# Kernel optimization log

Measured on AMD Instinct MI355X. Metric: run time of the kernel, lower is better.

## Reference

```python
import jax, jax.numpy as jnp
import numpy as np

NODE, CLUSTER, IN_DIM, OUT_DIM = 2048, 32, 64, 64
BATCH = 32

def _xavier_uniform(key, shape):
    fan_in, fan_out = shape[0], shape[1]
    limit = float(np.sqrt(6.0 / (fan_in + fan_out)))
    return jax.random.uniform(key, shape, jnp.float32, -limit, limit)

def setup_inputs() -> dict:
    key = jax.random.key(0)
    k_a, k_h, k_al, k_be = jax.random.split(key, 4)
    a = jax.random.uniform(k_a, (BATCH, NODE, NODE), jnp.float32)
    h = jax.random.normal(k_h, (BATCH, NODE, IN_DIM), jnp.float32)
    alpha = _xavier_uniform(k_al, (NODE, CLUSTER))
    beta = _xavier_uniform(k_be, (CLUSTER, IN_DIM * OUT_DIM))
    bias = jnp.zeros((OUT_DIM,), jnp.float32)
    return {"a": a, "h": h, "alpha": alpha, "beta": beta, "bias": bias}

def reference(a, h, alpha, beta, bias):
    # Low-rank per-node weight generation: (node, cluster) @ (cluster, in*out)
    w = (alpha @ beta).reshape(NODE, IN_DIM, OUT_DIM)
    # Per-node small matmul: h[b,n,:] @ w[n] + bias  -> (B, node, out)
    h2 = jnp.einsum('bni,nio->bno', h, w) + bias
    # Adjacency mixing with residual: a @ h2 + h2
    return jnp.einsum('bnm,bmo->bno', a, h2) + h2
```

## Files before the change

### kernel.cpp

```cpp
#include <hip/hip_runtime.h>

#define NODE 2048
#define KDIM 2048
#define CLUSTER 32
#define IN_DIM 64
#define OUT_DIM 64
#define BATCH 32

typedef short short8 __attribute__((ext_vector_type(8)));
typedef short short4v __attribute__((ext_vector_type(4)));
typedef float f32x4 __attribute__((ext_vector_type(4)));

__device__ __forceinline__ short f2bf(float f) {
  unsigned u = __float_as_uint(f);
  u += 0x7fffu + ((u >> 16) & 1u);
  return (short)(u >> 16);
}
__device__ __forceinline__ float bf2f(short s) {
  return __uint_as_float(((unsigned)(unsigned short)s) << 16);
}

typedef __attribute__((address_space(1))) const unsigned int gu32;
typedef __attribute__((address_space(3))) unsigned int lu32;
__device__ __forceinline__ void gl16nt(const void* g, void* l) {
  __builtin_amdgcn_global_load_lds((gu32*)g, (lu32*)l, 16, 0, 2);
}

__global__ __launch_bounds__(256) void k1_wgen(
    const float* __restrict__ alpha, const float* __restrict__ beta,
    short8* __restrict__ w_frag) {
  const int bid = blockIdx.x;
  const int ngrp = bid >> 1;
  const int ihalf = bid & 1;
  const int t = threadIdx.x;
  const int o = t & 63;
  const int igl = t >> 6;
  const int i0 = ihalf * 32 + igl * 8;
  const int n0 = ngrp * 8;

  float acc[8][8];
#pragma unroll
  for (int r = 0; r < 8; ++r)
#pragma unroll
    for (int j = 0; j < 8; ++j) acc[r][j] = 0.f;

  for (int k = 0; k < CLUSTER; ++k) {
    float av[8];
#pragma unroll
    for (int r = 0; r < 8; ++r) av[r] = alpha[(n0 + r) * CLUSTER + k];
    const float* bp = beta + k * (IN_DIM * OUT_DIM) + i0 * OUT_DIM + o;
#pragma unroll
    for (int j = 0; j < 8; ++j) {
      float bv = bp[j * OUT_DIM];
#pragma unroll
      for (int r = 0; r < 8; ++r) acc[r][j] += av[r] * bv;
    }
  }
#pragma unroll
  for (int r = 0; r < 8; ++r) {
    short8 s;
#pragma unroll
    for (int j = 0; j < 8; ++j) s[j] = f2bf(acc[r][j]);
    w_frag[((n0 + r) * 8 + (i0 >> 3)) * 64 + o] = s;
  }
}

__global__ __launch_bounds__(64) void k2_h2(
    const float* __restrict__ h, const short8* __restrict__ w_frag,
    const float* __restrict__ bias, short* __restrict__ h2_frag) {
  const int n = blockIdx.x;
  const int l = threadIdx.x;
  const int lr = l & 15, lk = l >> 4;

  short8 afr[2][2];
#pragma unroll
  for (int m = 0; m < 2; ++m)
#pragma unroll
    for (int kf = 0; kf < 2; ++kf) {
      const float* hp =
          h + ((size_t)(m * 16 + lr) * NODE + n) * IN_DIM + kf * 32 + lk * 8;
      f32x4 v0 = *(const f32x4*)hp;
      f32x4 v1 = *(const f32x4*)(hp + 4);
      short8 s;
#pragma unroll
      for (int j = 0; j < 4; ++j) { s[j] = f2bf(v0[j]); s[j + 4] = f2bf(v1[j]); }
      afr[m][kf] = s;
    }

  short8 bfr[4][2];
#pragma unroll
  for (int ng = 0; ng < 4; ++ng)
#pragma unroll
    for (int kf = 0; kf < 2; ++kf)
      bfr[ng][kf] = w_frag[(n * 8 + kf * 4 + lk) * 64 + ng * 16 + lr];

  f32x4 acc[2][4];
#pragma unroll
  for (int m = 0; m < 2; ++m)
#pragma unroll
    for (int ng = 0; ng < 4; ++ng) acc[m][ng] = (f32x4){0.f, 0.f, 0.f, 0.f};

#pragma unroll
  for (int kf = 0; kf < 2; ++kf)
#pragma unroll
    for (int m = 0; m < 2; ++m)
#pragma unroll
      for (int ng = 0; ng < 4; ++ng)
        acc[m][ng] = __builtin_amdgcn_mfma_f32_16x16x32_bf16(
            afr[m][kf], bfr[ng][kf], acc[m][ng], 0, 0, 0);

#pragma unroll
  for (int m = 0; m < 2; ++m)
#pragma unroll
    for (int ng = 0; ng < 4; ++ng) {
      const int o = ng * 16 + lr;
      const float bv = bias[o];
#pragma unroll
      for (int r = 0; r < 4; ++r) {
        const int b = m * 16 + lk * 4 + r;
        h2_frag[(((size_t)b * 256 + (n >> 3)) * 64 + o) * 8 + (n & 7)] =
            f2bf(acc[m][ng][r] + bv);
      }
    }
}

__global__ __launch_bounds__(256, 4) void k3_main(
    const float* __restrict__ a, const short* __restrict__ h2f,
    float* __restrict__ out) {
  __shared__ float lds[4][2][1024];
  const int bid0 = blockIdx.x;
  const int swz = (bid0 & 7) * 64 + (bid0 >> 3);
  const int b = swz >> 4;
  const int rt = swz & 15;
  const int t = threadIdx.x;
  const int wid = t >> 6;
  const int l = t & 63;
  const int lr = l & 15, lk = l >> 4;
  const int sw = l & 7;
  const int rowbase = rt * 128 + wid * 32;
  const int s0 = ((swz * 4 + wid) * 37) & 63;

  const char* gA = (const char*)(a + (size_t)b * NODE * KDIM
                                   + (size_t)(rowbase + (l >> 3)) * KDIM)
                   + (size_t)(((l & 7) ^ (l >> 3)) * 16);
  const short8* bbase = (const short8*)h2f + ((size_t)b * 256 + lk) * 64 + lr;

  char* ldsb0 = (char*)&lds[wid][0][0];
  char* ldsb1 = (char*)&lds[wid][1][0];
  const int O00 = lr * 128 + ((2 * lk + 0) ^ sw) * 16;
  const int O01 = lr * 128 + ((2 * lk + 1) ^ sw) * 16;
  const int O10 = (16 + lr) * 128 + ((2 * lk + 0) ^ sw) * 16;
  const int O11 = (16 + lr) * 128 + ((2 * lk + 1) ^ sw) * 16;

  f32x4 acc[2][4];
#pragma unroll
  for (int m = 0; m < 2; ++m)
#pragma unroll
    for (int ng = 0; ng < 4; ++ng) acc[m][ng] = (f32x4){0.f, 0.f, 0.f, 0.f};

  short8 BE[4], BO[4];

#define ISSUE_A(s, LP)                                   \
  do {                                                   \
    const int ss_ = ((s) + s0) & 63;                     \
    const char* g_ = gA + (size_t)ss_ * 128;             \
    gl16nt(g_ + 0 * 65536, (LP) + 0 * 1024);             \
    gl16nt(g_ + 1 * 65536, (LP) + 1 * 1024);             \
    gl16nt(g_ + 2 * 65536, (LP) + 2 * 1024);             \
    gl16nt(g_ + 3 * 65536, (LP) + 3 * 1024);             \
  } while (0)

#define ISSUE_B(s, BR)                                   \
  do {                                                   \
    const int ss_ = ((s) + s0) & 63;                     \
    const short8* q_ = bbase + ss_ * 256;                \
    BR[0] = q_[0];                                       \
    BR[1] = q_[16];                                      \
    BR[2] = q_[32];                                      \
    BR[3] = q_[48];                                      \
  } while (0)

#define COMPUTE(LP, BR)                                                     \
  do {                                                                      \
    f32x4 m0h0 = *(const f32x4*)((LP) + O00);                               \
    f32x4 m0h1 = *(const f32x4*)((LP) + O01);                               \
    f32x4 m1h0 = *(const f32x4*)((LP) + O10);                               \
    f32x4 m1h1 = *(const f32x4*)((LP) + O11);                               \
    short8 af0, af1;                                                        \
    _Pragma("unroll") for (int j_ = 0; j_ < 4; ++j_) {                      \
      af0[j_] = f2bf(m0h0[j_]);                                             \
      af0[j_ + 4] = f2bf(m0h1[j_]);                                         \
      af1[j_] = f2bf(m1h0[j_]);                                             \
      af1[j_ + 4] = f2bf(m1h1[j_]);                                         \
    }                                                                       \
    _Pragma("unroll") for (int ng_ = 0; ng_ < 4; ++ng_) {                   \
      acc[0][ng_] = __builtin_amdgcn_mfma_f32_16x16x32_bf16(                \
          af0, BR[ng_], acc[0][ng_], 0, 0, 0);                              \
      acc[1][ng_] = __builtin_amdgcn_mfma_f32_16x16x32_bf16(                \
          af1, BR[ng_], acc[1][ng_], 0, 0, 0);                              \
    }                                                                       \
  } while (0)

  ISSUE_A(0, ldsb0);
  ISSUE_B(0, BE);

#pragma unroll 1
  for (int u = 0; u < 32; ++u) {
    ISSUE_A(2 * u + 1, ldsb1);
    ISSUE_B(2 * u + 1, BO);
    asm volatile("s_waitcnt vmcnt(8)" ::: "memory");
    __builtin_amdgcn_sched_barrier(0);
    COMPUTE(ldsb0, BE);
    if (u < 31) {
      ISSUE_A(2 * u + 2, ldsb0);
      ISSUE_B(2 * u + 2, BE);
      asm volatile("s_waitcnt vmcnt(8)" ::: "memory");
    } else {
      asm volatile("s_waitcnt vmcnt(0)" ::: "memory");
    }
    __builtin_amdgcn_sched_barrier(0);
    COMPUTE(ldsb1, BO);
  }
#undef ISSUE_A
#undef ISSUE_B
#undef COMPUTE

#pragma unroll
  for (int m = 0; m < 2; ++m) {
    const int row0 = rowbase + m * 16 + lk * 4;
#pragma unroll
    for (int ng = 0; ng < 4; ++ng) {
      const int col = ng * 16 + lr;
      const short4v rv = *(const short4v*)&h2f[
          (((size_t)b * 256 + (row0 >> 3)) * 64 + col) * 8 + (row0 & 7)];
#pragma unroll
      for (int r = 0; r < 4; ++r) {
        out[((size_t)b * NODE + row0 + r) * 64 + col] =
            acc[m][ng][r] + bf2f(rv[r]);
      }
    }
  }
}

extern "C" void kernel_launch(void* const* d_in, const int* in_sizes, int n_in,
                              void* d_out, int out_size, void* d_ws, size_t ws_size,
                              hipStream_t stream) {
  const float* a     = (const float*)d_in[0];
  const float* h     = (const float*)d_in[1];
  const float* alpha = (const float*)d_in[2];
  const float* beta  = (const float*)d_in[3];
  const float* bias  = (const float*)d_in[4];
  float* out = (float*)d_out;

  short8* w_frag = (short8*)d_ws;
  short*  h2_frag = (short*)((char*)d_ws + (size_t)(16u << 20));

  k1_wgen<<<dim3(512), dim3(256), 0, stream>>>(alpha, beta, w_frag);
  k2_h2 <<<dim3(NODE), dim3(64),  0, stream>>>(h, w_frag, bias, h2_frag);
  k3_main<<<dim3(512), dim3(256), 0, stream>>>(a, h2_frag, out);
}
```

Baseline: 138.4 us.

## Fuse weight generation and per-node matmul into one kernel via LDS

Merges the low-rank weight generation kernel and the per-node h@W kernel into a single kernel. Each block builds bf16 weight fragments for 8 nodes in shared memory, then four waves each compute h2 for two nodes straight from LDS. This removes the 16 MB global round trip for w and one kernel launch. The cost is a smaller grid (256 blocks instead of 512 and 2048) and serialized loops inside each block, which may reduce parallelism.

```diff
diff --git a/kernel.cpp b/kernel.cpp
--- a/kernel.cpp
+++ b/kernel.cpp
@@ -26,102 +26,106 @@
   __builtin_amdgcn_global_load_lds((gu32*)g, (lu32*)l, 16, 0, 2);
 }
 
-__global__ __launch_bounds__(256) void k1_wgen(
+__global__ __launch_bounds__(256) void k12_wh2(
     const float* __restrict__ alpha, const float* __restrict__ beta,
-    short8* __restrict__ w_frag) {
+    const float* __restrict__ h, const float* __restrict__ bias,
+    short* __restrict__ h2_frag) {
+  __shared__ short8 w_lds[4096];
   const int bid = blockIdx.x;
-  const int ngrp = bid >> 1;
-  const int ihalf = bid & 1;
+  const int n0 = bid * 8;
   const int t = threadIdx.x;
   const int o = t & 63;
-  const int igl = t >> 6;
-  const int i0 = ihalf * 32 + igl * 8;
-  const int n0 = ngrp * 8;
-
-  float acc[8][8];
-#pragma unroll
-  for (int r = 0; r < 8; ++r)
-#pragma unroll
-    for (int j = 0; j < 8; ++j) acc[r][j] = 0.f;
-
-  for (int k = 0; k < CLUSTER; ++k) {
-    float av[8];
-#pragma unroll
-    for (int r = 0; r < 8; ++r) av[r] = alpha[(n0 + r) * CLUSTER + k];
-    const float* bp = beta + k * (IN_DIM * OUT_DIM) + i0 * OUT_DIM + o;
-#pragma unroll
-    for (int j = 0; j < 8; ++j) {
-      float bv = bp[j * OUT_DIM];
-#pragma unroll
-      for (int r = 0; r < 8; ++r) acc[r][j] += av[r] * bv;
-    }
-  }
-#pragma unroll
-  for (int r = 0; r < 8; ++r) {
-    short8 s;
-#pragma unroll
-    for (int j = 0; j < 8; ++j) s[j] = f2bf(acc[r][j]);
-    w_frag[((n0 + r) * 8 + (i0 >> 3)) * 64 + o] = s;
-  }
-}
-
-__global__ __launch_bounds__(64) void k2_h2(
-    const float* __restrict__ h, const short8* __restrict__ w_frag,
-    const float* __restrict__ bias, short* __restrict__ h2_frag) {
-  const int n = blockIdx.x;
-  const int l = threadIdx.x;
+  const int wid = t >> 6;
+
+#pragma unroll 1
+  for (int ihalf = 0; ihalf < 2; ++ihalf) {
+    const int i0 = ihalf * 32 + wid * 8;
+    float acc[8][8];
+#pragma unroll
+    for (int r = 0; r < 8; ++r)
+#pragma unroll
+      for (int j = 0; j < 8; ++j) acc[r][j] = 0.f;
+
+    for (int k = 0; k < CLUSTER; ++k) {
+      float av[8];
+#pragma unroll
+      for (int r = 0; r < 8; ++r) av[r] = alpha[(n0 + r) * CLUSTER + k];
+      const float* bp = beta + k * (IN_DIM * OUT_DIM) + i0 * OUT_DIM + o;
+#pragma unroll
+      for (int j = 0; j < 8; ++j) {
+        float bv = bp[j * OUT_DIM];
+#pragma unroll
+        for (int r = 0; r < 8; ++r) acc[r][j] += av[r] * bv;
+      }
+    }
+#pragma unroll
+    for (int r = 0; r < 8; ++r) {
+      short8 s;
+#pragma unroll
+      for (int j = 0; j < 8; ++j) s[j] = f2bf(acc[r][j]);
+      w_lds[(r * 8 + (i0 >> 3)) * 64 + o] = s;
+    }
+  }
+  __syncthreads();
+
+  const int l = t & 63;
   const int lr = l & 15, lk = l >> 4;
-
-  short8 afr[2][2];
-#pragma unroll
-  for (int m = 0; m < 2; ++m)
-#pragma unroll
-    for (int kf = 0; kf < 2; ++kf) {
-      const float* hp =
-          h + ((size_t)(m * 16 + lr) * NODE + n) * IN_DIM + kf * 32 + lk * 8;
-      f32x4 v0 = *(const f32x4*)hp;
-      f32x4 v1 = *(const f32x4*)(hp + 4);
-      short8 s;
-#pragma unroll
-      for (int j = 0; j < 4; ++j) { s[j] = f2bf(v0[j]); s[j + 4] = f2bf(v1[j]); }
-      afr[m][kf] = s;
-    }
-
-  short8 bfr[4][2];
-#pragma unroll
-  for (int ng = 0; ng < 4; ++ng)
+#pragma unroll 1
+  for (int rl = 0; rl < 2; ++rl) {
+    const int rloc = wid * 2 + rl;
+    const int n = n0 + rloc;
+
+    short8 afr[2][2];
+#pragma unroll
+    for (int m = 0; m < 2; ++m)
+#pragma unroll
+      for (int kf = 0; kf < 2; ++kf) {
+        const float* hp =
+            h + ((size_t)(m * 16 + lr) * NODE + n) * IN_DIM + kf * 32 + lk * 8;
+        f32x4 v0 = *(const f32x4*)hp;
+        f32x4 v1 = *(const f32x4*)(hp + 4);
+        short8 s;
+#pragma unroll
+        for (int j = 0; j < 4; ++j) { s[j] = f2bf(v0[j]); s[j + 4] = f2bf(v1[j]); }
+        afr[m][kf] = s;
+      }
+
+    short8 bfr[4][2];
+#pragma unroll
+    for (int ng = 0; ng < 4; ++ng)
+#pragma unroll
+      for (int kf = 0; kf < 2; ++kf)
+        bfr[ng][kf] = w_lds[(rloc * 8 + kf * 4 + lk) * 64 + ng * 16 + lr];
+
+    f32x4 acc[2][4];
+#pragma unroll
+    for (int m = 0; m < 2; ++m)
+#pragma unroll
+      for (int ng = 0; ng < 4; ++ng) acc[m][ng] = (f32x4){0.f, 0.f, 0.f, 0.f};
+
 #pragma unroll
     for (int kf = 0; kf < 2; ++kf)
-      bfr[ng][kf] = w_frag[(n * 8 + kf * 4 + lk) * 64 + ng * 16 + lr];
-
-  f32x4 acc[2][4];
-#pragma unroll
-  for (int m = 0; m < 2; ++m)
-#pragma unroll
-    for (int ng = 0; ng < 4; ++ng) acc[m][ng] = (f32x4){0.f, 0.f, 0.f, 0.f};
-
-#pragma unroll
-  for (int kf = 0; kf < 2; ++kf)
+#pragma unroll
+      for (int m = 0; m < 2; ++m)
+#pragma unroll
+        for (int ng = 0; ng < 4; ++ng)
+          acc[m][ng] = __builtin_amdgcn_mfma_f32_16x16x32_bf16(
+              afr[m][kf], bfr[ng][kf], acc[m][ng], 0, 0, 0);
+
 #pragma unroll
     for (int m = 0; m < 2; ++m)
 #pragma unroll
-      for (int ng = 0; ng < 4; ++ng)
-        acc[m][ng] = __builtin_amdgcn_mfma_f32_16x16x32_bf16(
-            afr[m][kf], bfr[ng][kf], acc[m][ng], 0, 0, 0);
-
-#pragma unroll
-  for (int m = 0; m < 2; ++m)
-#pragma unroll
-    for (int ng = 0; ng < 4; ++ng) {
-      const int o = ng * 16 + lr;
-      const float bv = bias[o];
-#pragma unroll
-      for (int r = 0; r < 4; ++r) {
-        const int b = m * 16 + lk * 4 + r;
-        h2_frag[(((size_t)b * 256 + (n >> 3)) * 64 + o) * 8 + (n & 7)] =
-            f2bf(acc[m][ng][r] + bv);
-      }
-    }
+      for (int ng = 0; ng < 4; ++ng) {
+        const int oo = ng * 16 + lr;
+        const float bv = bias[oo];
+#pragma unroll
+        for (int r = 0; r < 4; ++r) {
+          const int b = m * 16 + lk * 4 + r;
+          h2_frag[(((size_t)b * 256 + (n >> 3)) * 64 + oo) * 8 + (n & 7)] =
+              f2bf(acc[m][ng][r] + bv);
+        }
+      }
+  }
 }
 
 __global__ __launch_bounds__(256, 4) void k3_main(
@@ -252,10 +256,8 @@
   const float* bias  = (const float*)d_in[4];
   float* out = (float*)d_out;
 
-  short8* w_frag = (short8*)d_ws;
-  short*  h2_frag = (short*)((char*)d_ws + (size_t)(16u << 20));
-
-  k1_wgen<<<dim3(512), dim3(256), 0, stream>>>(alpha, beta, w_frag);
-  k2_h2 <<<dim3(NODE), dim3(64),  0, stream>>>(h, w_frag, bias, h2_frag);
+  short* h2_frag = (short*)((char*)d_ws + (size_t)(16u << 20));
+
+  k12_wh2<<<dim3(256), dim3(256), 0, stream>>>(alpha, beta, h, bias, h2_frag);
   k3_main<<<dim3(512), dim3(256), 0, stream>>>(a, h2_frag, out);
 }
```

Result: faster. 133.3 us (-3.7%).
